# Optimization experiments

Measured on AMD Instinct MI355X. Metric: run time of the kernel, lower is better.

The kernel has to match this reference:

```python
import jax, jax.numpy as jnp
import numpy as np

B, T, D, H = 2048, 250, 128, 100

def setup_inputs() -> dict:
    key = jax.random.key(0)
    k1, k2, k3, k4 = jax.random.split(key, 4)
    x = jax.random.normal(k1, (B, T, D), dtype=jnp.float32)
    # fused LSTM kernels, gate order (i, f, g, o); scale for stability
    Wi = jax.random.normal(k2, (D, 4 * H), dtype=jnp.float32) * 0.05
    Wh = jax.random.normal(k3, (H, 4 * H), dtype=jnp.float32) * 0.05
    bh = jnp.zeros((4 * H,), dtype=jnp.float32)
    Wd = jax.random.normal(k4, (H, H), dtype=jnp.float32) * 0.05
    bd = jnp.zeros((H,), dtype=jnp.float32)
    return {"x": x, "Wi": Wi, "Wh": Wh, "bh": bh, "Wd": Wd, "bd": bd}

def reference(x, Wi, Wh, bh, Wd, bd):
    b = x.shape[0]
    # precompute input contribution for all timesteps: [B, T, 4H]
    xz = jnp.einsum('btd,dg->btg', x, Wi) + bh

    def step(carry, xz_t):
        c, h = carry
        z = xz_t + h @ Wh                      # [B, 4H]
        i, f, g, o = jnp.split(z, 4, axis=-1)  # flax gate order i,f,g,o
        i = jax.nn.sigmoid(i)
        f = jax.nn.sigmoid(f)
        g = jnp.tanh(g)
        o = jax.nn.sigmoid(o)
        c = f * c + i * g
        h = o * jnp.tanh(c)
        return (c, h), h

    c0 = jnp.zeros((b, H), dtype=x.dtype)
    h0 = jnp.zeros((b, H), dtype=x.dtype)
    _, hs = jax.lax.scan(step, (c0, h0), jnp.swapaxes(xz, 0, 1))
    hs = jnp.swapaxes(hs, 0, 1)                # [B, T, H]
    return jax.nn.relu(hs @ Wd + bd)
```

## Files before the change

kernel.cpp:

```cpp
#include <hip/hip_runtime.h>

#define TPB 448

typedef __attribute__((ext_vector_type(8))) short bf16x8;
typedef __attribute__((ext_vector_type(4))) float f32x4;

__device__ __forceinline__ short f2bf(float f) {
    union { float f; unsigned u; } v; v.f = f;
    unsigned r = (v.u + 0x7FFFu + ((v.u >> 16) & 1u)) >> 16;
    return (short)r;
}

__device__ __forceinline__ float frcp(float x) {
#if __has_builtin(__builtin_amdgcn_rcpf)
    return __builtin_amdgcn_rcpf(x);
#else
    return 1.0f / x;
#endif
}

__device__ __forceinline__ float fast_sig(float x) {
    return frcp(1.0f + __expf(-x));
}
__device__ __forceinline__ float fast_tanh(float x) {
    return 1.0f - 2.0f * frcp(1.0f + __expf(2.0f * x));
}

__device__ __forceinline__ float permlane_pack(float a, float b) {
#if __has_builtin(__builtin_amdgcn_permlane32_swap)
    auto r = __builtin_amdgcn_permlane32_swap(__float_as_int(a), __float_as_int(b),
                                              false, false);
    return __int_as_float(r[0]);
#else
    const int l  = (int)(threadIdx.x & 63);
    const int bs = __shfl(__float_as_int(b), l ^ 32, 64);
    return __int_as_float(l >= 32 ? bs : __float_as_int(a));
#endif
}

__device__ __forceinline__ void block_sync_lds() {
    asm volatile("s_waitcnt lgkmcnt(0)\n\ts_barrier" ::: "memory");
}

__global__ __launch_bounds__(TPB, 2) void lstm_fused_all(
    const float* __restrict__ x,
    const float* __restrict__ Wi,
    const float* __restrict__ Wh,
    const float* __restrict__ bh,
    const float* __restrict__ Wd,
    const float* __restrict__ bd,
    float* __restrict__ out)
{
    const int tid  = threadIdx.x;
    const int lane = tid & 63;
    const int wave = tid >> 6;
    const int m16  = lane & 15;
    const int kg   = lane >> 4;
    const int b0   = blockIdx.x * 8;

    __shared__ short xA[3][16 * 136];
    __shared__ short hA[2][16 * 136];

    for (int i = tid; i < 3 * 16 * 136; i += TPB) ((short*)xA)[i] = 0;
    for (int i = tid; i < 2 * 16 * 136; i += TPB) ((short*)hA)[i] = 0;

    const int  cg    = wave * 16 + m16;
    const bool valid = (cg < 100);

    bf16x8 bWi[4][4], bWh[4][4], bWd[4];
    float  bhv[4];
    #pragma unroll
    for (int G = 0; G < 4; ++G) {
        const int c = G * 100 + cg;
        bhv[G] = valid ? bh[c] : 0.0f;
        #pragma unroll
        for (int s = 0; s < 4; ++s) {
            bf16x8 vi, vh;
            #pragma unroll
            for (int j = 0; j < 8; ++j) {
                const int k = s * 32 + kg * 8 + j;
                vi[j] = f2bf(valid ? Wi[k * 400 + c] : 0.0f);
                vh[j] = f2bf((valid && k < 100) ? Wh[k * 400 + c] : 0.0f);
            }
            bWi[G][s] = vi;
            bWh[G][s] = vh;
        }
    }
    const float bdv = valid ? bd[cg] : 0.0f;
    #pragma unroll
    for (int s = 0; s < 4; ++s) {
        bf16x8 vd;
        #pragma unroll
        for (int j = 0; j < 8; ++j) {
            const int k = s * 32 + kg * 8 + j;
            vd[j] = f2bf((valid && k < 100) ? Wd[k * 100 + cg] : 0.0f);
        }
        bWd[s] = vd;
    }

    const int kgq     = (lane >> 4) & 1;
    const int rowbase = kgq * 4 + ((lane >= 32) ? 2 : 0);
    float myC[2] = {0.f, 0.f};
    long  ob2[2];
    #pragma unroll
    for (int j = 0; j < 2; ++j)
        ob2[j] = (long)(b0 + rowbase + j) * 25000 + cg;

    const long xb0 = ((long)(b0 + wave) * 250) * 128 + lane * 2;
    const long xb1 = ((long)(b0 + 7)    * 250) * 128 + lane * 2;
    float2 la0, la1 = {0.f, 0.f}, lb0, lb1 = {0.f, 0.f};
    la0 = *(const float2*)&x[xb0];
    if (wave == 0) la1 = *(const float2*)&x[xb1];
    lb0 = *(const float2*)&x[xb0 + 128];
    if (wave == 0) lb1 = *(const float2*)&x[xb1 + 128];

    const int aoff = m16 * 136 + kg * 8;

    __syncthreads();

    {
        short2 s0; s0.x = f2bf(la0.x); s0.y = f2bf(la0.y);
        *(short2*)&xA[0][wave * 136 + lane * 2] = s0;
        if (wave == 0) {
            short2 s1; s1.x = f2bf(la1.x); s1.y = f2bf(la1.y);
            *(short2*)&xA[0][7 * 136 + lane * 2] = s1;
        }
    }
    __syncthreads();
    la0 = lb0; if (wave == 0) la1 = lb1;
    lb0 = *(const float2*)&x[xb0 + 2 * 128];
    if (wave == 0) lb1 = *(const float2*)&x[xb1 + 2 * 128];

    f32x4 accI[4];
    {
        bf16x8 aX[4];
        #pragma unroll
        for (int s = 0; s < 4; ++s)
            aX[s] = *(const bf16x8*)&xA[0][aoff + s * 32];
        #pragma unroll
        for (int G = 0; G < 4; ++G) {
            const f32x4 a = {bhv[G], bhv[G], bhv[G], bhv[G]};
            accI[G] = a;
        }
        #pragma unroll
        for (int s = 0; s < 4; ++s)
            #pragma unroll
            for (int G = 0; G < 4; ++G)
                accI[G] = __builtin_amdgcn_mfma_f32_16x16x32_bf16(aX[s], bWi[G][s], accI[G], 0, 0, 0);
    }

    int  bufx = 1;
    int  ooff = 0;
    long xoff = 3 * 128;

    #pragma unroll 1
    for (int t = 0; t <= 250; ++t) {
        const int bufh = t & 1;

        if (t + 1 < 250) {
            short2 s0; s0.x = f2bf(la0.x); s0.y = f2bf(la0.y);
            *(short2*)&xA[bufx][wave * 136 + lane * 2] = s0;
            if (wave == 0) {
                short2 s1; s1.x = f2bf(la1.x); s1.y = f2bf(la1.y);
                *(short2*)&xA[bufx][7 * 136 + lane * 2] = s1;
            }
        }
        block_sync_lds();

        if (t + 1 < 250) { la0 = lb0; if (wave == 0) la1 = lb1; }
        if (t + 3 < 250) {
            lb0 = *(const float2*)&x[xb0 + xoff];
            if (wave == 0) lb1 = *(const float2*)&x[xb1 + xoff];
        }
        xoff += 128;

        bf16x8 aH[4];
        #pragma unroll
        for (int s = 0; s < 4; ++s)
            aH[s] = *(const bf16x8*)&hA[bufh][aoff + s * 32];

        if (t < 250) {
            f32x4 accH0[4], accH1[4];
            #pragma unroll
            for (int G = 0; G < 4; ++G) {
                const f32x4 zz = {0.f, 0.f, 0.f, 0.f};
                accH0[G] = __builtin_amdgcn_mfma_f32_16x16x32_bf16(aH[0], bWh[G][0], zz, 0, 0, 0);
                accH1[G] = __builtin_amdgcn_mfma_f32_16x16x32_bf16(aH[2], bWh[G][2], zz, 0, 0, 0);
            }
            #pragma unroll
            for (int G = 0; G < 4; ++G) {
                accH0[G] = __builtin_amdgcn_mfma_f32_16x16x32_bf16(aH[1], bWh[G][1], accH0[G], 0, 0, 0);
                accH1[G] = __builtin_amdgcn_mfma_f32_16x16x32_bf16(aH[3], bWh[G][3], accH1[G], 0, 0, 0);
            }

            float z0[4], z1[4];
            #pragma unroll
            for (int G = 0; G < 4; ++G) {
                const f32x4 zs = accI[G] + (accH0[G] + accH1[G]);
                z0[G] = permlane_pack(zs[0], zs[2]);
                z1[G] = permlane_pack(zs[1], zs[3]);
            }
            if (valid) {
                {
                    const float ig = fast_sig(z0[0]);
                    const float fg = fast_sig(z0[1]);
                    const float gg = fast_tanh(z0[2]);
                    const float og = fast_sig(z0[3]);
                    const float cs = fg * myC[0] + ig * gg;
                    myC[0] = cs;
                    const float h = og * fast_tanh(cs);
                    hA[bufh ^ 1][(rowbase + 0) * 136 + cg] = f2bf(h);
                }
                {
                    const float ig = fast_sig(z1[0]);
                    const float fg = fast_sig(z1[1]);
                    const float gg = fast_tanh(z1[2]);
                    const float og = fast_sig(z1[3]);
                    const float cs = fg * myC[1] + ig * gg;
                    myC[1] = cs;
                    const float h = og * fast_tanh(cs);
                    hA[bufh ^ 1][(rowbase + 1) * 136 + cg] = f2bf(h);
                }
            }
        }

        if (t + 1 < 250) {
            bf16x8 aX[4];
            #pragma unroll
            for (int s = 0; s < 4; ++s)
                aX[s] = *(const bf16x8*)&xA[bufx][aoff + s * 32];
            #pragma unroll
            for (int G = 0; G < 4; ++G) {
                const f32x4 a = {bhv[G], bhv[G], bhv[G], bhv[G]};
                accI[G] = a;
            }
            #pragma unroll
            for (int s = 0; s < 4; ++s)
                #pragma unroll
                for (int G = 0; G < 4; ++G)
                    accI[G] = __builtin_amdgcn_mfma_f32_16x16x32_bf16(aX[s], bWi[G][s], accI[G], 0, 0, 0);
            bufx = (bufx == 2) ? 0 : bufx + 1;
        }

        if (t > 0) {
            f32x4 oacc = {bdv, bdv, bdv, bdv};
            #pragma unroll
            for (int s = 0; s < 4; ++s)
                oacc = __builtin_amdgcn_mfma_f32_16x16x32_bf16(aH[s], bWd[s], oacc, 0, 0, 0);
            const float o0 = permlane_pack(oacc[0], oacc[2]);
            const float o1 = permlane_pack(oacc[1], oacc[3]);
            if (valid) {
                out[ob2[0] + ooff] = o0 > 0.0f ? o0 : 0.0f;
                out[ob2[1] + ooff] = o1 > 0.0f ? o1 : 0.0f;
            }
            ooff += 100;
        }
    }
}

extern "C" void kernel_launch(void* const* d_in, const int* in_sizes, int n_in,
                              void* d_out, int out_size, void* d_ws, size_t ws_size,
                              hipStream_t stream) {
    (void)in_sizes; (void)n_in; (void)out_size; (void)d_ws; (void)ws_size;
    const float* x  = (const float*)d_in[0];
    const float* Wi = (const float*)d_in[1];
    const float* Wh = (const float*)d_in[2];
    const float* bh = (const float*)d_in[3];
    const float* Wd = (const float*)d_in[4];
    const float* bd = (const float*)d_in[5];
    float* out = (float*)d_out;

    lstm_fused_all<<<256, TPB, 0, stream>>>(x, Wi, Wh, bh, Wd, bd, out);
}
```

Baseline: 679.7 us.

## Halve batch rows per block to launch twice as many blocks

Each block now handles 4 batch rows instead of 8, and the grid doubles from 256 to 512 blocks. Only waves 0-3 stage x rows into shared memory, and lanes for rows beyond 4 skip the gate math and the output stores. The aim is to fill more compute units and shorten each block's serial 250-step recurrence by spreading it across more parallel blocks. The cost is that MFMA tiles are now half-empty, so total matrix work and weight loads per output double.

```diff
diff --git a/kernel.cpp b/kernel.cpp
--- a/kernel.cpp
+++ b/kernel.cpp
@@ -1,6 +1,7 @@
 #include <hip/hip_runtime.h>
 
-#define TPB 448
+#define TPB  448
+#define ROWS 4
 
 typedef __attribute__((ext_vector_type(8))) short bf16x8;
 typedef __attribute__((ext_vector_type(4))) float f32x4;
@@ -56,7 +57,7 @@
     const int wave = tid >> 6;
     const int m16  = lane & 15;
     const int kg   = lane >> 4;
-    const int b0   = blockIdx.x * 8;
+    const int b0   = blockIdx.x * ROWS;
 
     __shared__ short xA[3][16 * 136];
     __shared__ short hA[2][16 * 136];
@@ -98,38 +99,36 @@
         bWd[s] = vd;
     }
 
-    const int kgq     = (lane >> 4) & 1;
-    const int rowbase = kgq * 4 + ((lane >= 32) ? 2 : 0);
+    const int  kgq     = (lane >> 4) & 1;
+    const int  rowbase = kgq * 4 + ((lane >= 32) ? 2 : 0);
+    const bool rowv    = (rowbase < ROWS);
     float myC[2] = {0.f, 0.f};
     long  ob2[2];
     #pragma unroll
     for (int j = 0; j < 2; ++j)
-        ob2[j] = (long)(b0 + rowbase + j) * 25000 + cg;
-
-    const long xb0 = ((long)(b0 + wave) * 250) * 128 + lane * 2;
-    const long xb1 = ((long)(b0 + 7)    * 250) * 128 + lane * 2;
-    float2 la0, la1 = {0.f, 0.f}, lb0, lb1 = {0.f, 0.f};
-    la0 = *(const float2*)&x[xb0];
-    if (wave == 0) la1 = *(const float2*)&x[xb1];
-    lb0 = *(const float2*)&x[xb0 + 128];
-    if (wave == 0) lb1 = *(const float2*)&x[xb1 + 128];
+        ob2[j] = (long)(b0 + (rowv ? rowbase + j : 0)) * 25000 + cg;
+
+    const bool stager = (wave < ROWS);
+    const long xb0 = ((long)(b0 + (stager ? wave : 0)) * 250) * 128 + lane * 2;
+    float2 la0 = {0.f, 0.f}, lb0 = {0.f, 0.f};
+    if (stager) {
+        la0 = *(const float2*)&x[xb0];
+        lb0 = *(const float2*)&x[xb0 + 128];
+    }
 
     const int aoff = m16 * 136 + kg * 8;
 
     __syncthreads();
 
-    {
+    if (stager) {
         short2 s0; s0.x = f2bf(la0.x); s0.y = f2bf(la0.y);
         *(short2*)&xA[0][wave * 136 + lane * 2] = s0;
-        if (wave == 0) {
-            short2 s1; s1.x = f2bf(la1.x); s1.y = f2bf(la1.y);
-            *(short2*)&xA[0][7 * 136 + lane * 2] = s1;
-        }
     }
     __syncthreads();
-    la0 = lb0; if (wave == 0) la1 = lb1;
-    lb0 = *(const float2*)&x[xb0 + 2 * 128];
-    if (wave == 0) lb1 = *(const float2*)&x[xb1 + 2 * 128];
+    if (stager) {
+        la0 = lb0;
+        lb0 = *(const float2*)&x[xb0 + 2 * 128];
+    }
 
     f32x4 accI[4];
     {
@@ -157,20 +156,15 @@
     for (int t = 0; t <= 250; ++t) {
         const int bufh = t & 1;
 
-        if (t + 1 < 250) {
+        if (stager && t + 1 < 250) {
             short2 s0; s0.x = f2bf(la0.x); s0.y = f2bf(la0.y);
             *(short2*)&xA[bufx][wave * 136 + lane * 2] = s0;
-            if (wave == 0) {
-                short2 s1; s1.x = f2bf(la1.x); s1.y = f2bf(la1.y);
-                *(short2*)&xA[bufx][7 * 136 + lane * 2] = s1;
-            }
         }
         block_sync_lds();
 
-        if (t + 1 < 250) { la0 = lb0; if (wave == 0) la1 = lb1; }
-        if (t + 3 < 250) {
-            lb0 = *(const float2*)&x[xb0 + xoff];
-            if (wave == 0) lb1 = *(const float2*)&x[xb1 + xoff];
+        if (stager) {
+            if (t + 1 < 250) la0 = lb0;
+            if (t + 3 < 250) lb0 = *(const float2*)&x[xb0 + xoff];
         }
         xoff += 128;
 
@@ -200,7 +194,7 @@
                 z0[G] = permlane_pack(zs[0], zs[2]);
                 z1[G] = permlane_pack(zs[1], zs[3]);
             }
-            if (valid) {
+            if (valid && rowv) {
                 {
                     const float ig = fast_sig(z0[0]);
                     const float fg = fast_sig(z0[1]);
@@ -249,7 +243,7 @@
                 oacc = __builtin_amdgcn_mfma_f32_16x16x32_bf16(aH[s], bWd[s], oacc, 0, 0, 0);
             const float o0 = permlane_pack(oacc[0], oacc[2]);
             const float o1 = permlane_pack(oacc[1], oacc[3]);
-            if (valid) {
+            if (valid && rowv) {
                 out[ob2[0] + ooff] = o0 > 0.0f ? o0 : 0.0f;
                 out[ob2[1] + ooff] = o1 > 0.0f ? o1 : 0.0f;
             }
@@ -270,5 +264,5 @@
     const float* bd = (const float*)d_in[5];
     float* out = (float*)d_out;
 
-    lstm_fused_all<<<256, TPB, 0, stream>>>(x, Wi, Wh, bh, Wd, bd, out);
-}
+    lstm_fused_all<<<2048 / ROWS, TPB, 0, stream>>>(x, Wi, Wh, bh, Wd, bd, out);
+}
```

Result: slower. 1.047 ms (+54.0%).
